# Performance work log

Hardware: AMD Instinct MI355X
Metric: run time of the kernel (lower is better)

## Reference

```python
import jax, jax.numpy as jnp
import numpy as np
from jax import lax

SOBEL_X = jnp.array([[-1., 0., 1.], [-2., 0., 2.], [-1., 0., 1.]], jnp.float32).reshape(1, 1, 3, 3)
SOBEL_Y = jnp.array([[1., 2., 1.], [0., 0., 0.], [-1., -2., -1.]], jnp.float32).reshape(1, 1, 3, 3)


def _edge_detect(img):
    dn = ('NCHW', 'OIHW', 'NCHW')
    ex = lax.conv_general_dilated(img, SOBEL_X, (1, 1), [(1, 1), (1, 1)], dimension_numbers=dn)
    ey = lax.conv_general_dilated(img, SOBEL_Y, (1, 1), [(1, 1), (1, 1)], dimension_numbers=dn)
    return jnp.abs(ex) + jnp.abs(ey)


def _point_sample(img, pts):
    # img [B,C,H,W], pts [B,N,2] in [0,1] (x=width first). Matches torch
    # F.grid_sample(img, 2*pts-1, bilinear, align_corners=False, zero padding).
    B, C, H, W = img.shape
    g = 2.0 * pts - 1.0
    gx = ((g[..., 0] + 1.0) * W - 1.0) * 0.5
    gy = ((g[..., 1] + 1.0) * H - 1.0) * 0.5
    x0 = jnp.floor(gx)
    y0 = jnp.floor(gy)
    wx1 = gx - x0
    wy1 = gy - y0
    flat = img.reshape(B, C, H * W)
    Np = pts.shape[1]

    def gather(xi, yi):
        valid = (xi >= 0) & (xi <= W - 1) & (yi >= 0) & (yi <= H - 1)
        xi_c = jnp.clip(xi, 0, W - 1).astype(jnp.int32)
        yi_c = jnp.clip(yi, 0, H - 1).astype(jnp.int32)
        lin = yi_c * W + xi_c  # [B,N]
        idx = jnp.broadcast_to(lin[:, None, :], (B, C, Np))
        return jnp.take_along_axis(flat, idx, axis=2) * valid[:, None, :]

    v = ((1 - wx1) * (1 - wy1))[:, None, :] * gather(x0, y0) \
        + (wx1 * (1 - wy1))[:, None, :] * gather(x0 + 1, y0) \
        + ((1 - wx1) * wy1)[:, None, :] * gather(x0, y0 + 1) \
        + (wx1 * wy1)[:, None, :] * gather(x0 + 1, y0 + 1)
    return v  # [B,C,N]


def _ln(x, g, b, eps=1e-5):
    m = jnp.mean(x, axis=-1, keepdims=True)
    v = jnp.mean((x - m) ** 2, axis=-1, keepdims=True)
    return (x - m) * lax.rsqrt(v + eps) * g + b


def _sampling_points(out, N, over_gen, rand_point, beta=0.75):
    # torch version is @torch.no_grad()
    out = lax.stop_gradient(out)
    B = out.shape[0]
    n_imp = int(beta * N)
    sorted_mask = -jnp.sort(-out, axis=1)  # sort channels descending
    og_map = _point_sample(sorted_mask, over_gen)  # [B,C,k*N]
    unc = -(og_map[:, 0] - og_map[:, 1])
    _, idx = lax.top_k(unc, n_imp)
    importance = jnp.take_along_axis(over_gen, idx[..., None], axis=1)  # [B,n_imp,2]
    edge_num = (N - n_imp) // 2
    crack = jax.nn.softmax(out, axis=1)[:, 1:2]
    edge = _edge_detect(crack)
    eh, ew = edge.shape[-2], edge.shape[-1]
    _, eidx = lax.top_k(edge.reshape(B, -1), edge_num)
    # Faithful to torch: float division results are copied back into a long
    # tensor, truncating toward zero (these coords collapse to 0 since idx < h*w).
    c0 = jnp.trunc(eidx.astype(jnp.float32) / ew / eh)
    c1 = jnp.trunc((eidx % ew).astype(jnp.float32) / ew)
    coverage = jnp.stack([c0, c1], axis=-1)
    return jnp.concatenate([importance, coverage, rand_point], axis=1)  # [B,N,2]


def setup_inputs() -> dict:
    key = jax.random.key(0)
    ks = jax.random.split(key, 12)
    B, in_c, C, Hx, Hf = 8, 512, 2, 1024, 128
    N = Hx // 8  # 128
    n_imp = int(0.75 * N)  # 96
    edge_num = (N - n_imp) // 2  # 16
    rand_num = N - n_imp - edge_num  # 16
    x = jax.random.normal(ks[0], (B, 3, Hx, Hx), jnp.float32)
    res2 = jax.random.normal(ks[1], (B, in_c, Hf, Hf), jnp.float32)
    out = jax.random.normal(ks[2], (B, C, Hf, Hf), jnp.float32)
    over_gen = jax.random.uniform(ks[3], (B, 3 * N, 2), jnp.float32)
    rand_point = jax.random.uniform(ks[4], (B, rand_num, 2), jnp.float32)
    dropout_mask = (jax.random.uniform(ks[5], (B, C, N)) > 0.2).astype(jnp.float32) / 0.8
    std = 0.02
    h2 = in_c // 2
    w1 = jax.random.normal(ks[6], (in_c + C, in_c), jnp.float32) * std
    w2 = jax.random.normal(ks[7], (in_c, h2), jnp.float32) * std
    w3 = jax.random.normal(ks[8], (h2, C), jnp.float32) * std
    return {"x": x, "res2": res2, "out": out, "over_gen": over_gen,
            "rand_point": rand_point, "dropout_mask": dropout_mask,
            "w1": w1, "b1": jnp.zeros(in_c), "g1": jnp.ones(in_c), "be1": jnp.zeros(in_c),
            "w2": w2, "b2": jnp.zeros(h2), "g2": jnp.ones(h2), "be2": jnp.zeros(h2),
            "w3": w3, "b3": jnp.zeros(C)}


def reference(x, res2, out, over_gen, rand_point, dropout_mask,
              w1, b1, g1, be1, w2, b2, g2, be2, w3, b3):
    N = x.shape[-1] // 8
    points = _sampling_points(out, N, over_gen, rand_point)  # [B,N,2]
    coarse = _point_sample(out, points)   # [B,C,N]
    fine = _point_sample(res2, points)    # [B,in_c,N]
    feat = jnp.concatenate([coarse, fine], axis=1).transpose(0, 2, 1)  # [B,N,in_c+C]
    h = jax.nn.gelu(_ln(feat @ w1 + b1, g1, be1), approximate=False)
    h = jax.nn.gelu(_ln(h @ w2 + b2, g2, be2), approximate=False)
    pred = (h @ w3 + b3).transpose(0, 2, 1)  # [B,C,N]
    rend = pred * dropout_mask + coarse  # Dropout(0.2) as explicit mask
    return rend, points
```

## Files before the change

kernel.cpp:

```cpp
#include <hip/hip_runtime.h>
#include <cstddef>

#pragma clang fp contract(off)

struct Samp {
    int o00, o01, o10, o11;
    float w00, w01, w10, w11;
};
__device__ __forceinline__ float grid_coord(float p) {
    float g = 2.0f * p - 1.0f;
    return ((g + 1.0f) * 128.0f - 1.0f) * 0.5f;
}
__device__ __forceinline__ Samp mk_samp(float px, float py) {
    Samp s;
    float gx = grid_coord(px);
    float gy = grid_coord(py);
    float x0f = floorf(gx), y0f = floorf(gy);
    float wx1 = gx - x0f, wy1 = gy - y0f;
    float wx0 = 1.0f - wx1, wy0 = 1.0f - wy1;
    int x0 = (int)x0f, y0 = (int)y0f;
    int x1 = x0 + 1, y1 = y0 + 1;
    bool vx0 = (x0 >= 0) && (x0 < 128);
    bool vx1 = (x1 >= 0) && (x1 < 128);
    bool vy0 = (y0 >= 0) && (y0 < 128);
    bool vy1 = (y1 >= 0) && (y1 < 128);
    s.o00 = (vx0 && vy0) ? (y0 * 128 + x0) : -1;
    s.o01 = (vx1 && vy0) ? (y0 * 128 + x1) : -1;
    s.o10 = (vx0 && vy1) ? (y1 * 128 + x0) : -1;
    s.o11 = (vx1 && vy1) ? (y1 * 128 + x1) : -1;
    s.w00 = wx0 * wy0; s.w01 = wx1 * wy0;
    s.w10 = wx0 * wy1; s.w11 = wx1 * wy1;
    return s;
}
__device__ __forceinline__ float samp_apply(const float* __restrict__ img, const Samp& s) {
    float v00 = (s.o00 >= 0) ? img[s.o00] : 0.f;
    float v01 = (s.o01 >= 0) ? img[s.o01] : 0.f;
    float v10 = (s.o10 >= 0) ? img[s.o10] : 0.f;
    float v11 = (s.o11 >= 0) ? img[s.o11] : 0.f;
    return ((s.w00 * v00 + s.w01 * v01) + s.w10 * v10) + s.w11 * v11;
}
__device__ __forceinline__ float gelu_exact(float h) {
    return 0.5f * h * (1.f + erff(h * 0.70710678118654752f));
}

__global__ __launch_bounds__(384) void k_points(
    const float* __restrict__ out, const float* __restrict__ over_gen,
    const float* __restrict__ rand_point,
    float* __restrict__ d_out, float* __restrict__ pts_ws, float* __restrict__ coarse_ws)
{
    int b = blockIdx.x;
    int tid = threadIdx.x;
    __shared__ float unc[384];
    __shared__ float pts[128][2];
    size_t outbase = (size_t)b * 2 * 16384;
    float px = over_gen[(size_t)(b * 384 + tid) * 2 + 0];
    float py = over_gen[(size_t)(b * 384 + tid) * 2 + 1];
    {
        Samp s = mk_samp(px, py);
        float M00 = 0.f, M01 = 0.f, M10 = 0.f, M11 = 0.f;
        float m00 = 0.f, m01 = 0.f, m10 = 0.f, m11 = 0.f;
        if (s.o00 >= 0) { float a = out[outbase + s.o00], c = out[outbase + 16384 + s.o00]; M00 = fmaxf(a, c); m00 = fminf(a, c); }
        if (s.o01 >= 0) { float a = out[outbase + s.o01], c = out[outbase + 16384 + s.o01]; M01 = fmaxf(a, c); m01 = fminf(a, c); }
        if (s.o10 >= 0) { float a = out[outbase + s.o10], c = out[outbase + 16384 + s.o10]; M10 = fmaxf(a, c); m10 = fminf(a, c); }
        if (s.o11 >= 0) { float a = out[outbase + s.o11], c = out[outbase + 16384 + s.o11]; M11 = fmaxf(a, c); m11 = fminf(a, c); }
        float og0 = ((s.w00 * M00 + s.w01 * M01) + s.w10 * M10) + s.w11 * M11;
        float og1 = ((s.w00 * m00 + s.w01 * m01) + s.w10 * m10) + s.w11 * m11;
        unc[tid] = og1 - og0;
    }
    __syncthreads();
    {
        float v = unc[tid];
        int rank = 0;
        for (int j = 0; j < 384; ++j) {
            float u = unc[j];
            rank += (u > v) || (u == v && j < tid);
        }
        if (rank < 96) { pts[rank][0] = px; pts[rank][1] = py; }
    }
    if (tid < 16) {
        pts[96 + tid][0] = 0.f; pts[96 + tid][1] = 0.f;
    } else if (tid < 32) {
        int r = tid - 16;
        pts[112 + r][0] = rand_point[(size_t)(b * 16 + r) * 2 + 0];
        pts[112 + r][1] = rand_point[(size_t)(b * 16 + r) * 2 + 1];
    }
    __syncthreads();
    if (tid < 128) {
        float qx = pts[tid][0], qy = pts[tid][1];
        pts_ws[(b * 128 + tid) * 2 + 0] = qx;
        pts_ws[(b * 128 + tid) * 2 + 1] = qy;
        d_out[2048 + (size_t)(b * 128 + tid) * 2 + 0] = qx;
        d_out[2048 + (size_t)(b * 128 + tid) * 2 + 1] = qy;
    }
    if (tid < 256) {
        int c = tid >> 7, n = tid & 127;
        Samp s = mk_samp(pts[n][0], pts[n][1]);
        coarse_ws[(b * 2 + c) * 128 + n] = samp_apply(out + (size_t)(b * 2 + c) * 16384, s);
    }
}

#define ROWS 4
__global__ __launch_bounds__(512) void k_fused(
    const float* __restrict__ res2, const float* __restrict__ pts_ws,
    const float* __restrict__ coarse_ws,
    const float* __restrict__ w1, const float* __restrict__ b1,
    const float* __restrict__ g1, const float* __restrict__ be1,
    const float* __restrict__ w2, const float* __restrict__ b2,
    const float* __restrict__ g2, const float* __restrict__ be2,
    const float* __restrict__ w3, const float* __restrict__ b3,
    const float* __restrict__ mask, float* __restrict__ d_out)
{
    __shared__ float feat[ROWS][514];
    __shared__ float h1s[ROWS][512];
    __shared__ float h2s[ROWS][256];
    __shared__ float part2[256][ROWS];
    __shared__ float pd[8][32];
    __shared__ float red_s[8][ROWS], red_q[8][ROWS];
    __shared__ float stat_m[ROWS], stat_r[ROWS];
    __shared__ float ptsl[ROWS][2];

    int blk = blockIdx.x;
    int b = blk >> 5, n0 = (blk & 31) * ROWS;
    int tid = threadIdx.x;
    int wave = tid >> 6, lane = tid & 63;

    if (tid < ROWS * 2)
        ((float*)ptsl)[tid] = pts_ws[(size_t)(b * 128 + n0) * 2 + tid];
    if (tid >= 64 && tid < 64 + ROWS * 2) {
        int i = tid - 64, r = i >> 1, c = i & 1;
        feat[r][c] = coarse_ws[(b * 2 + c) * 128 + (n0 + r)];
    }
    __syncthreads();

#pragma unroll
    for (int r = 0; r < ROWS; ++r) {
        Samp s = mk_samp(ptsl[r][0], ptsl[r][1]);
        const float* img = res2 + ((size_t)(b * 512 + tid) << 14);
        feat[r][2 + tid] = samp_apply(img, s);
    }
    __syncthreads();

    int col = tid;
    float acc1[ROWS] = {0.f, 0.f, 0.f, 0.f};
    for (int k = 0; k < 514; ++k) {
        float w = w1[(size_t)k * 512 + col];
#pragma unroll
        for (int r = 0; r < ROWS; ++r) acc1[r] = fmaf(feat[r][k], w, acc1[r]);
    }
    {
        float bb = b1[col], ga = g1[col], ea = be1[col];
        float v[ROWS];
#pragma unroll
        for (int r = 0; r < ROWS; ++r) v[r] = acc1[r] + bb;
#pragma unroll
        for (int r = 0; r < ROWS; ++r) {
            float s = v[r], q = v[r] * v[r];
            for (int off = 32; off > 0; off >>= 1) {
                s += __shfl_down(s, off, 64);
                q += __shfl_down(q, off, 64);
            }
            if (lane == 0) { red_s[wave][r] = s; red_q[wave][r] = q; }
        }
        __syncthreads();
        if (tid < ROWS) {
            float s = 0.f, q = 0.f;
            for (int w8 = 0; w8 < 8; ++w8) { s += red_s[w8][tid]; q += red_q[w8][tid]; }
            float m = s * (1.f / 512.f);
            float var = q * (1.f / 512.f) - m * m;
            stat_m[tid] = m;
            stat_r[tid] = 1.f / sqrtf(var + 1e-5f);
        }
        __syncthreads();
#pragma unroll
        for (int r = 0; r < ROWS; ++r)
            h1s[r][col] = gelu_exact((v[r] - stat_m[r]) * stat_r[r] * ga + ea);
    }
    __syncthreads();

    int c2 = tid & 255, kh = tid >> 8;
    float acc2[ROWS] = {0.f, 0.f, 0.f, 0.f};
    for (int k = 0; k < 256; ++k) {
        int kk = (kh << 8) + k;
        float w = w2[(size_t)kk * 256 + c2];
#pragma unroll
        for (int r = 0; r < ROWS; ++r) acc2[r] = fmaf(h1s[r][kk], w, acc2[r]);
    }
    if (kh == 1) {
#pragma unroll
        for (int r = 0; r < ROWS; ++r) part2[c2][r] = acc2[r];
    }
    __syncthreads();
    float v2[ROWS];
    float ga2 = 0.f, ea2 = 0.f;
    if (kh == 0) {
        float bb2 = b2[c2];
        ga2 = g2[c2]; ea2 = be2[c2];
#pragma unroll
        for (int r = 0; r < ROWS; ++r) {
            v2[r] = (acc2[r] + part2[c2][r]) + bb2;
            float s = v2[r], q = v2[r] * v2[r];
            for (int off = 32; off > 0; off >>= 1) {
                s += __shfl_down(s, off, 64);
                q += __shfl_down(q, off, 64);
            }
            if (lane == 0) { red_s[wave][r] = s; red_q[wave][r] = q; }
        }
    }
    __syncthreads();
    if (tid < ROWS) {
        float s = 0.f, q = 0.f;
        for (int w4 = 0; w4 < 4; ++w4) { s += red_s[w4][tid]; q += red_q[w4][tid]; }
        float m = s * (1.f / 256.f);
        float var = q * (1.f / 256.f) - m * m;
        stat_m[tid] = m;
        stat_r[tid] = 1.f / sqrtf(var + 1e-5f);
    }
    __syncthreads();
    if (kh == 0) {
#pragma unroll
        for (int r = 0; r < ROWS; ++r)
            h2s[r][c2] = gelu_exact((v2[r] - stat_m[r]) * stat_r[r] * ga2 + ea2);
    }
    __syncthreads();

    if (tid < 256) {
        int rc = tid >> 5, l = tid & 31;
        int r = rc >> 1, c = rc & 1;
        float p = 0.f;
        for (int k = l; k < 256; k += 32) p = fmaf(h2s[r][k], w3[k * 2 + c], p);
        pd[rc][l] = p;
    }
    __syncthreads();
    if (tid < 8) {
        int r = tid >> 1, c = tid & 1;
        float acc = 0.f;
        for (int l = 0; l < 32; ++l) acc += pd[tid][l];
        float pred = acc + b3[c];
        int oi = b * 256 + c * 128 + (n0 + r);
        d_out[oi] = pred * mask[oi] + coarse_ws[oi];
    }
}

extern "C" void kernel_launch(void* const* d_in, const int* in_sizes, int n_in,
                              void* d_out, int out_size, void* d_ws, size_t ws_size,
                              hipStream_t stream) {
    const float* res2 = (const float*)d_in[1];
    const float* out  = (const float*)d_in[2];
    const float* over_gen   = (const float*)d_in[3];
    const float* rand_point = (const float*)d_in[4];
    const float* mask = (const float*)d_in[5];
    const float* w1 = (const float*)d_in[6];
    const float* b1 = (const float*)d_in[7];
    const float* g1 = (const float*)d_in[8];
    const float* be1 = (const float*)d_in[9];
    const float* w2 = (const float*)d_in[10];
    const float* b2 = (const float*)d_in[11];
    const float* g2 = (const float*)d_in[12];
    const float* be2 = (const float*)d_in[13];
    const float* w3 = (const float*)d_in[14];
    const float* b3 = (const float*)d_in[15];
    float* o = (float*)d_out;

    float* fws = (float*)d_ws;
    float* pts_ws    = fws;
    float* coarse_ws = fws + 2048;

    k_points<<<8, 384, 0, stream>>>(out, over_gen, rand_point, o, pts_ws, coarse_ws);
    k_fused<<<8 * 32, 512, 0, stream>>>(res2, pts_ws, coarse_ws,
                                        w1, b1, g1, be1, w2, b2, g2, be2, w3, b3,
                                        mask, o);
}
```

Before: 510.1 us.

## Replace scattered res2 bilinear gathers with a full streaming pass and scatter lists

New measurement: 594.1 us. +16.5%, slower.

```diff
diff --git a/kernel.cpp b/kernel.cpp
--- a/kernel.cpp
+++ b/kernel.cpp
@@ -99,9 +99,49 @@
     }
 }
 
+__global__ __launch_bounds__(512) void k_slots(
+    const float* __restrict__ pts_ws, float* __restrict__ wgt4,
+    int* __restrict__ head, int* __restrict__ nxt)
+{
+    int b = blockIdx.x, tid = threadIdx.x;
+    int4* h4 = (int4*)(head + b * 16384);
+    int4 m1; m1.x = m1.y = m1.z = m1.w = -1;
+    for (int i = tid; i < 4096; i += 512) h4[i] = m1;
+    __syncthreads();
+    int n = tid >> 2, nb = tid & 3;
+    float px = pts_ws[(b * 128 + n) * 2 + 0];
+    float py = pts_ws[(b * 128 + n) * 2 + 1];
+    Samp s = mk_samp(px, py);
+    int   o = (nb == 0) ? s.o00 : (nb == 1) ? s.o01 : (nb == 2) ? s.o10 : s.o11;
+    float w = (nb == 0) ? s.w00 : (nb == 1) ? s.w01 : (nb == 2) ? s.w10 : s.w11;
+    wgt4[(b * 128 + n) * 4 + nb] = (o >= 0) ? w : 0.0f;
+    if (o >= 0) nxt[b * 512 + tid] = atomicExch(&head[b * 16384 + o], tid);
+}
+
+__global__ __launch_bounds__(256) void k_stream(
+    const float* __restrict__ res2, const int* __restrict__ head,
+    const int* __restrict__ nxt, float* __restrict__ cols)
+{
+    size_t t = (size_t)blockIdx.x * 256 + threadIdx.x;
+    int q  = (int)(t & 4095);
+    int bc = (int)(t >> 12);
+    int b  = bc >> 9;
+    int ch = bc & 511;
+    const int4 h4 = ((const int4*)(head + b * 16384))[q];
+    float4 v = ((const float4*)res2)[t];
+    asm volatile("" :: "v"(v.x), "v"(v.y), "v"(v.z), "v"(v.w));
+    float* colb = cols + ((size_t)b << 18) + ch;
+    const int* nx = nxt + (b << 9);
+    int e;
+    e = h4.x; while (e >= 0) { colb[(size_t)e << 9] = v.x; e = nx[e]; }
+    e = h4.y; while (e >= 0) { colb[(size_t)e << 9] = v.y; e = nx[e]; }
+    e = h4.z; while (e >= 0) { colb[(size_t)e << 9] = v.z; e = nx[e]; }
+    e = h4.w; while (e >= 0) { colb[(size_t)e << 9] = v.w; e = nx[e]; }
+}
+
 #define ROWS 4
-__global__ __launch_bounds__(512) void k_fused(
-    const float* __restrict__ res2, const float* __restrict__ pts_ws,
+__global__ __launch_bounds__(512) void k_mlp(
+    const float* __restrict__ cols, const float* __restrict__ wgt4,
     const float* __restrict__ coarse_ws,
     const float* __restrict__ w1, const float* __restrict__ b1,
     const float* __restrict__ g1, const float* __restrict__ be1,
@@ -117,26 +157,22 @@
     __shared__ float pd[8][32];
     __shared__ float red_s[8][ROWS], red_q[8][ROWS];
     __shared__ float stat_m[ROWS], stat_r[ROWS];
-    __shared__ float ptsl[ROWS][2];
 
     int blk = blockIdx.x;
     int b = blk >> 5, n0 = (blk & 31) * ROWS;
     int tid = threadIdx.x;
     int wave = tid >> 6, lane = tid & 63;
 
-    if (tid < ROWS * 2)
-        ((float*)ptsl)[tid] = pts_ws[(size_t)(b * 128 + n0) * 2 + tid];
-    if (tid >= 64 && tid < 64 + ROWS * 2) {
-        int i = tid - 64, r = i >> 1, c = i & 1;
+    if (tid < ROWS * 2) {
+        int r = tid >> 1, c = tid & 1;
         feat[r][c] = coarse_ws[(b * 2 + c) * 128 + (n0 + r)];
     }
-    __syncthreads();
-
 #pragma unroll
     for (int r = 0; r < ROWS; ++r) {
-        Samp s = mk_samp(ptsl[r][0], ptsl[r][1]);
-        const float* img = res2 + ((size_t)(b * 512 + tid) << 14);
-        feat[r][2 + tid] = samp_apply(img, s);
+        const float4 wg = ((const float4*)wgt4)[b * 128 + n0 + r];
+        const float* basep = cols + ((size_t)b << 18) + (size_t)((n0 + r) * 4) * 512 + tid;
+        float v00 = basep[0], v01 = basep[512], v10 = basep[1024], v11 = basep[1536];
+        feat[r][2 + tid] = ((wg.x * v00 + wg.y * v01) + wg.z * v10) + wg.w * v11;
     }
     __syncthreads();
 
@@ -263,10 +299,16 @@
 
     float* fws = (float*)d_ws;
     float* pts_ws    = fws;
-    float* coarse_ws = fws + 2048;
+    float* coarse_ws = pts_ws + 2048;
+    float* wgt4      = coarse_ws + 2048;
+    float* cols      = wgt4 + 4096;
+    int*   head      = (int*)(cols + (8 << 18));
+    int*   nxt       = head + 8 * 16384;
 
     k_points<<<8, 384, 0, stream>>>(out, over_gen, rand_point, o, pts_ws, coarse_ws);
-    k_fused<<<8 * 32, 512, 0, stream>>>(res2, pts_ws, coarse_ws,
-                                        w1, b1, g1, be1, w2, b2, g2, be2, w3, b3,
-                                        mask, o);
-}
+    k_slots<<<8, 512, 0, stream>>>(pts_ws, wgt4, head, nxt);
+    k_stream<<<65536, 256, 0, stream>>>(res2, head, nxt, cols);
+    k_mlp<<<256, 512, 0, stream>>>(cols, wgt4, coarse_ws,
+                                   w1, b1, g1, be1, w2, b2, g2, be2, w3, b3,
+                                   mask, o);
+}
```
